# Kernel optimization log

Hardware: AMD Instinct MI355X
Metric: run time of the kernel (lower is better)

Reference implementation:

```python
import jax, jax.numpy as jnp
import numpy as np

B, S, E, H = 8, 1024, 1024, 16
D = E // H


def setup_inputs() -> dict:
    key = jax.random.key(0)
    ks = jax.random.split(key, 5)
    s = 1.0 / np.sqrt(E)
    return {
        "hidden_states": jax.random.normal(ks[0], (B, S, E), dtype=jnp.float32),
        "w_q": jax.random.normal(ks[1], (E, E), dtype=jnp.float32) * s,
        "w_k": jax.random.normal(ks[2], (E, E), dtype=jnp.float32) * s,
        "w_v": jax.random.normal(ks[3], (E, E), dtype=jnp.float32) * s,
        "w_out": jax.random.normal(ks[4], (E, E), dtype=jnp.float32) * s,
        "b_out": jnp.zeros((E,), dtype=jnp.float32),
    }


def reference(hidden_states, w_q, w_k, w_v, w_out, b_out):
    b, s = hidden_states.shape[0], hidden_states.shape[1]
    # Linear projections (weights stored as [in, out] = torch W^T)
    q = hidden_states @ w_q
    k = hidden_states @ w_k
    v = hidden_states @ w_v
    # Faithful to the original: raw reshape (B,S,E)->(B,H,S,D), NOT a head-split transpose
    q = q.reshape(b, H, s, D)
    k = k.reshape(b, H, s, D)
    v = v.reshape(b, H, s, D)
    # Scores scaled by embedding_size**-0.5 (original quirk, not head_dim**-0.5)
    scores = jnp.einsum("bhsd,bhtd->bhst", q, k) * (E ** -0.5)
    attn = jax.nn.softmax(scores, axis=-1)
    out = jnp.einsum("bhst,bhtd->bhsd", attn, v)  # [B,H,S,D]
    out = out.transpose(0, 2, 1, 3).reshape(b, s, E)  # [B,S,E]
    return out @ w_out + b_out
```

## Files before the change

### kernel.cpp

```cpp
#include <hip/hip_runtime.h>
#include <hip/hip_bf16.h>
#include <stdint.h>
#include <stddef.h>

static constexpr int Bb = 8, Ss = 1024, Ee = 1024, Hh = 16, Dd = 64;
static constexpr int Mm = Bb * Ss;

typedef __attribute__((ext_vector_type(8))) short frag8;
typedef __attribute__((ext_vector_type(4))) float fx4;
typedef __attribute__((ext_vector_type(4))) short s4v;

#define GP(p) ((const __attribute__((address_space(1))) void*)(p))
#define LP(p) ((__attribute__((address_space(3))) void*)(p))

static constexpr float QSC = 0.045084220027780106f;

__device__ inline short f2bf(float x) {
  union { float f; unsigned u; } c; c.f = x;
  unsigned u = c.u;
  unsigned r = (u + 0x7FFFu + ((u >> 16) & 1u)) >> 16;
  return (short)r;
}

__global__ __launch_bounds__(256) void cvt_kernel(const float* __restrict__ in,
                                                  short* __restrict__ out, int n4) {
  int i = blockIdx.x * 256 + threadIdx.x;
  if (i >= n4) return;
  float4 v = *((const float4*)in + i);
  union { short s[4]; uint2 u; } o;
  o.s[0] = f2bf(v.x); o.s[1] = f2bf(v.y); o.s[2] = f2bf(v.z); o.s[3] = f2bf(v.w);
  *(uint2*)(out + (size_t)i * 4) = o.u;
}

__global__ __launch_bounds__(256) void transpose_cvt4(const float* __restrict__ w0,
                                                      const float* __restrict__ w1,
                                                      const float* __restrict__ w2,
                                                      const float* __restrict__ w3,
                                                      short* __restrict__ WtBase) {
  __shared__ short tile[32][33];
  const int z = blockIdx.z;
  const float* W = z == 0 ? w0 : (z == 1 ? w1 : (z == 2 ? w2 : w3));
  short* Wt = WtBase + (size_t)z * 1024 * 1024;
  const int bx = blockIdx.x * 32;
  const int by = blockIdx.y * 32;
  const int tx = threadIdx.x & 31, ty = threadIdx.x >> 5;
  #pragma unroll
  for (int j = 0; j < 32; j += 8)
    tile[ty + j][tx] = f2bf(W[(size_t)(by + ty + j) * 1024 + bx + tx]);
  __syncthreads();
  #pragma unroll
  for (int j = 0; j < 32; j += 8)
    Wt[(size_t)(bx + ty + j) * 1024 + by + tx] = tile[tx][ty + j];
}

__global__ __launch_bounds__(256) void transpose_v(const short* __restrict__ V,
                                                   short* __restrict__ Vt) {
  __shared__ short tile[64][65];
  const int bh = blockIdx.y;
  const int s0 = blockIdx.x * 64;
  const short* Vb = V + (size_t)bh * 65536;
  short* Vtb = Vt + (size_t)bh * 65536;
  const int tx = threadIdx.x & 63, ty = threadIdx.x >> 6;
  #pragma unroll
  for (int j = 0; j < 64; j += 4)
    tile[ty + j][tx] = Vb[(size_t)(s0 + ty + j) * 64 + tx];
  __syncthreads();
  #pragma unroll
  for (int j = 0; j < 64; j += 4)
    Vtb[(size_t)(ty + j) * 1024 + s0 + tx] = tile[tx][ty + j];
}

template <int MODE>
__global__ __launch_bounds__(256) void gemm_bt(const short* __restrict__ A,
                                               const short* __restrict__ Bt,
                                               void* __restrict__ C0,
                                               void* __restrict__ C1,
                                               void* __restrict__ C2,
                                               const float* __restrict__ bias,
                                               int M, int N, int K) {
  __shared__ short As[128 * 32];
  __shared__ short Bs[128 * 32];
  const int t = threadIdx.x;
  const int w = t >> 6, lane = t & 63;
  const int fm = lane & 15, quad = lane >> 4;
  const int m0 = blockIdx.y * 128, n0 = blockIdx.x * 128;
  const int wm = (w >> 1) * 64, wn = (w & 1) * 64;
  fx4 acc[4][4];
  #pragma unroll
  for (int i = 0; i < 4; ++i)
    #pragma unroll
    for (int j = 0; j < 4; ++j) acc[i][j] = (fx4){0.f, 0.f, 0.f, 0.f};

  for (int k0 = 0; k0 < K; k0 += 32) {
    #pragma unroll
    for (int i = 0; i < 2; ++i) {
      int chunk = i * 256 + t;
      int row = chunk >> 2, cc = chunk & 3;
      __builtin_amdgcn_global_load_lds(GP(A + (size_t)(m0 + row) * K + k0 + cc * 8),
                                       LP(As + chunk * 8), 16, 0, 0);
      __builtin_amdgcn_global_load_lds(GP(Bt + (size_t)(n0 + row) * K + k0 + cc * 8),
                                       LP(Bs + chunk * 8), 16, 0, 0);
    }
    __syncthreads();
    frag8 af[4], bf[4];
    #pragma unroll
    for (int mt = 0; mt < 4; ++mt)
      af[mt] = *(const frag8*)(As + (wm + mt * 16 + fm) * 32 + quad * 8);
    #pragma unroll
    for (int nt = 0; nt < 4; ++nt)
      bf[nt] = *(const frag8*)(Bs + (wn + nt * 16 + fm) * 32 + quad * 8);
    #pragma unroll
    for (int mt = 0; mt < 4; ++mt)
      #pragma unroll
      for (int nt = 0; nt < 4; ++nt)
        acc[mt][nt] = __builtin_amdgcn_mfma_f32_16x16x32_bf16(af[mt], bf[nt], acc[mt][nt], 0, 0, 0);
    __syncthreads();
  }
  if (MODE == 0) {
    const int nb = n0 >> 10;
    short* dst = nb == 0 ? (short*)C0 : (nb == 1 ? (short*)C1 : (short*)C2);
    const float scl = (nb == 0) ? QSC : 1.0f;
    const int nl0 = n0 & 1023;
    #pragma unroll
    for (int mt = 0; mt < 4; ++mt)
      #pragma unroll
      for (int nt = 0; nt < 4; ++nt)
        #pragma unroll
        for (int r = 0; r < 4; ++r) {
          int row = m0 + wm + mt * 16 + quad * 4 + r;
          int col = nl0 + wn + nt * 16 + fm;
          dst[(size_t)row * 1024 + col] = f2bf(acc[mt][nt][r] * scl);
        }
  } else {
    #pragma unroll
    for (int mt = 0; mt < 4; ++mt)
      #pragma unroll
      for (int nt = 0; nt < 4; ++nt)
        #pragma unroll
        for (int r = 0; r < 4; ++r) {
          int row = m0 + wm + mt * 16 + quad * 4 + r;
          int col = n0 + wn + nt * 16 + fm;
          ((float*)C0)[(size_t)row * N + col] = acc[mt][nt][r] + bias[col];
        }
  }
}

__global__ __launch_bounds__(256, 2) void attn_kernel(const short* __restrict__ Q,
                                                      const short* __restrict__ K,
                                                      const short* __restrict__ Vt,
                                                      short* __restrict__ Ctx) {
  __shared__ short Ks[2][4096];
  __shared__ short Vs[2][4096];
  __shared__ short Plds[4 * 64 * 72];
  const int bh = blockIdx.x, qt = blockIdx.y;
  const int t = threadIdx.x;
  const int w = t >> 6, lane = t & 63;
  const int fm = lane & 15, quad = lane >> 4;
  const short* Qb = Q + (size_t)bh * 65536;
  const short* Kb = K + (size_t)bh * 65536;
  const short* Vb = Vt + (size_t)bh * 65536;
  const int q0 = qt * 256 + w * 64;
  short* myP = Plds + w * 4608;

  frag8 qb[4][2];
  #pragma unroll
  for (int g = 0; g < 4; ++g)
    #pragma unroll
    for (int h = 0; h < 2; ++h)
      qb[g][h] = *(const frag8*)(Qb + (size_t)(q0 + g * 16 + fm) * 64 + h * 32 + quad * 8);

  fx4 O[4][4];
  #pragma unroll
  for (int g = 0; g < 4; ++g)
    #pragma unroll
    for (int nt = 0; nt < 4; ++nt) O[g][nt] = (fx4){0.f, 0.f, 0.f, 0.f};
  float lp[4] = {0.f, 0.f, 0.f, 0.f};

  int koff[2], voff[2], loff[2];
  #pragma unroll
  for (int i = 0; i < 2; ++i) {
    int c = i * 256 + t;
    int cf = c & 15, cq = (c >> 4) & 3, ch = (c >> 6) & 1, cg = c >> 7;
    koff[i] = (cg * 16 + cf) * 64 + ch * 32 + cq * 8;
    voff[i] = (cg * 16 + cf) * 1024 + ch * 32 + cq * 8;
    loff[i] = c * 8;
  }

  #pragma unroll
  for (int i = 0; i < 2; ++i) {
    __builtin_amdgcn_global_load_lds(GP(Kb + koff[i]), LP(&Ks[0][0] + loff[i]), 16, 0, 0);
    __builtin_amdgcn_global_load_lds(GP(Vb + voff[i]), LP(&Vs[0][0] + loff[i]), 16, 0, 0);
  }
  __syncthreads();

  for (int c = 0; c < 16; ++c) {
    const int cur = c & 1;
    if (c < 15) {
      const int key0n = (c + 1) * 64;
      #pragma unroll
      for (int i = 0; i < 2; ++i) {
        __builtin_amdgcn_global_load_lds(GP(Kb + (size_t)key0n * 64 + koff[i]),
                                         LP(&Ks[cur ^ 1][0] + loff[i]), 16, 0, 0);
        __builtin_amdgcn_global_load_lds(GP(Vb + (size_t)key0n + voff[i]),
                                         LP(&Vs[cur ^ 1][0] + loff[i]), 16, 0, 0);
      }
    }
    const short* Kc = &Ks[cur][0];
    const short* Vc = &Vs[cur][0];

    #pragma unroll
    for (int s = 0; s < 4; ++s) {
      frag8 k0 = *(const frag8*)(Kc + (s * 2 + 0) * 512 + lane * 8);
      frag8 k1 = *(const frag8*)(Kc + (s * 2 + 1) * 512 + lane * 8);
      #pragma unroll
      for (int g = 0; g < 4; ++g) {
        fx4 z = (fx4){0.f, 0.f, 0.f, 0.f};
        z = __builtin_amdgcn_mfma_f32_16x16x32_bf16(k0, qb[g][0], z, 0, 0, 0);
        z = __builtin_amdgcn_mfma_f32_16x16x32_bf16(k1, qb[g][1], z, 0, 0, 0);
        s4v pv;
        #pragma unroll
        for (int r = 0; r < 4; ++r) {
          float p = __builtin_amdgcn_exp2f(z[r]);
          lp[g] += p;
          union { float f; unsigned u; } cv; cv.f = p;
          pv[r] = (short)(cv.u >> 16);
        }
        *(s4v*)(myP + (g * 16 + fm) * 72 + s * 16 + quad * 4) = pv;
      }
    }
    asm volatile("s_waitcnt lgkmcnt(0)" ::: "memory");
    #pragma unroll
    for (int h = 0; h < 2; ++h) {
      frag8 pf[4];
      #pragma unroll
      for (int g = 0; g < 4; ++g)
        pf[g] = *(const frag8*)(myP + (g * 16 + fm) * 72 + h * 32 + quad * 8);
      #pragma unroll
      for (int nt = 0; nt < 4; ++nt) {
        frag8 vf = *(const frag8*)(Vc + (nt * 2 + h) * 512 + lane * 8);
        #pragma unroll
        for (int g = 0; g < 4; ++g)
          O[g][nt] = __builtin_amdgcn_mfma_f32_16x16x32_bf16(pf[g], vf, O[g][nt], 0, 0, 0);
      }
    }
    __syncthreads();
  }

  float rl[4][4];
  #pragma unroll
  for (int g = 0; g < 4; ++g) {
    float v = lp[g];
    v += __shfl_xor(v, 16, 64);
    v += __shfl_xor(v, 32, 64);
    float inv = 1.f / v;
    #pragma unroll
    for (int r = 0; r < 4; ++r) rl[g][r] = __shfl(inv, quad * 4 + r, 16);
  }
  const int b = bh >> 4, h = bh & 15;
  #pragma unroll
  for (int g = 0; g < 4; ++g)
    #pragma unroll
    for (int nt = 0; nt < 4; ++nt)
      #pragma unroll
      for (int r = 0; r < 4; ++r) {
        int row = b * 1024 + q0 + g * 16 + quad * 4 + r;
        int col = h * 64 + nt * 16 + fm;
        Ctx[(size_t)row * 1024 + col] = f2bf(O[g][nt][r] * rl[g][r]);
      }
}

extern "C" void kernel_launch(void* const* d_in, const int* in_sizes, int n_in,
                              void* d_out, int out_size, void* d_ws, size_t ws_size,
                              hipStream_t stream) {
  const float* hs = (const float*)d_in[0];
  const float* wq = (const float*)d_in[1];
  const float* wk = (const float*)d_in[2];
  const float* wv = (const float*)d_in[3];
  const float* wo = (const float*)d_in[4];
  const float* bo = (const float*)d_in[5];
  float* out = (float*)d_out;

  char* wp = (char*)d_ws;
  const size_t MB16 = (size_t)Mm * Ee * 2;
  const size_t MB2  = (size_t)Ee * Ee * 2;
  short* Xb  = (short*)wp; wp += MB16;
  short* Wqt = (short*)wp; wp += MB2;
  short* Wkt = (short*)wp; wp += MB2;
  short* Wvt = (short*)wp; wp += MB2;
  short* Wot = (short*)wp; wp += MB2;
  short* Qb  = (short*)wp; wp += MB16;
  short* Kb  = (short*)wp; wp += MB16;
  short* Vb  = (short*)wp; wp += MB16;
  short* Vt  = (short*)wp; wp += MB16;
  short* Ctx = (short*)wp; wp += MB16;

  cvt_kernel<<<(Mm * Ee / 4 + 255) / 256, 256, 0, stream>>>(hs, Xb, Mm * Ee / 4);
  transpose_cvt4<<<dim3(32, 32, 4), 256, 0, stream>>>(wq, wk, wv, wo, Wqt);
  gemm_bt<0><<<dim3(24, 64), 256, 0, stream>>>(Xb, Wqt, Qb, Kb, Vb, nullptr, Mm, 3072, Ee);
  transpose_v<<<dim3(16, 128), 256, 0, stream>>>(Vb, Vt);
  attn_kernel<<<dim3(128, 4), 256, 0, stream>>>(Qb, Kb, Vt, Ctx);
  gemm_bt<1><<<dim3(8, 64), 256, 0, stream>>>(Ctx, Wot, out, nullptr, nullptr, bo, Mm, Ee, Ee);
}
```

Before: 251.2 us.

## Replace QKV projection GEMM with 256x256 double-buffered phased MFMA kernel

Adds a dedicated QKV projection kernel that uses 256x256 tiles, 512 threads and K=64 steps. Global-to-LDS loads are double-buffered and the next tile's prefetch is split across four MFMA phases with explicit vmcnt waits and barriers. It also applies an XOR swizzle to the LDS layout to avoid bank conflicts, remaps workgroups in groups of 8 for cache locality, and raises priority during MFMA bursts. The aim is to hide global memory latency and increase reuse per tile. In exchange it uses more LDS and registers per block, and correctness depends on the hand-tuned waitcnt counts.

```diff
diff --git a/kernel.cpp b/kernel.cpp
--- a/kernel.cpp
+++ b/kernel.cpp
@@ -68,6 +68,145 @@
   #pragma unroll
   for (int j = 0; j < 64; j += 4)
     Vtb[(size_t)(ty + j) * 1024 + s0 + tx] = tile[tx][ty + j];
+}
+
+__global__ __launch_bounds__(512, 2) void gemm_qkv_8ph(const short* __restrict__ A,
+                                                       const short* __restrict__ Bt,
+                                                       short* __restrict__ Cq,
+                                                       short* __restrict__ Ck,
+                                                       short* __restrict__ Cv) {
+  __shared__ short As[2][16384];
+  __shared__ short Bs[2][16384];
+  const int t = threadIdx.x;
+  const int w = t >> 6, lane = t & 63;
+  const int fm = lane & 15, quad = lane >> 4;
+  const int wm = w >> 1, wn = w & 1;
+  const int wg = (blockIdx.x & 7) * 48 + (blockIdx.x >> 3);
+  const int nt_i = wg % 12, mt_i = wg / 12;
+  const int m0 = mt_i * 256, n0 = nt_i * 256;
+
+  int goffA[4], goffB[4];
+  #pragma unroll
+  for (int i = 0; i < 4; ++i) {
+    int c = i * 512 + t, row = c >> 3, col8 = (c & 7) ^ (row & 7);
+    goffA[i] = row * 1024 + col8 * 8;
+  }
+  {
+    int row32 = (t >> 3) & 31, hv = t >> 8, col8 = (t & 7) ^ (row32 & 7);
+    #pragma unroll
+    for (int j = 0; j < 4; ++j)
+      goffB[j] = (hv * 128 + j * 32 + row32) * 1024 + col8 * 8;
+  }
+  const short* Ag = A + (size_t)m0 * 1024;
+  const short* Bg = Bt + (size_t)n0 * 1024;
+
+  fx4 acc[4][8];
+  #pragma unroll
+  for (int i = 0; i < 4; ++i)
+    #pragma unroll
+    for (int j = 0; j < 8; ++j) acc[i][j] = (fx4){0.f, 0.f, 0.f, 0.f};
+
+  const int s0o = ((0 * 4 + quad) ^ (fm & 7)) * 8;
+  const int s1o = ((1 * 4 + quad) ^ (fm & 7)) * 8;
+  const int aBase = (wm * 64 + fm) * 64;
+  const int bBase = wn * 2048 + fm * 64;
+
+#define STG_A(i, koff, dstbuf) \
+  __builtin_amdgcn_global_load_lds(GP(Ag + (koff) + goffA[i]), \
+                                   LP((dstbuf) + ((i) * 512 + t) * 8), 16, 0, 0)
+#define STG_B(j, koff, dstbuf) \
+  __builtin_amdgcn_global_load_lds(GP(Bg + (koff) + goffB[j]), \
+                                   LP((dstbuf) + ((j) * 512 + t) * 8), 16, 0, 0)
+#define LOAD_B(p) \
+  { const short* bp = Bb + (p) * 4096 + bBase; \
+    bf[0][0] = *(const frag8*)(bp + s0o); \
+    bf[0][1] = *(const frag8*)(bp + s1o); \
+    bf[1][0] = *(const frag8*)(bp + 1024 + s0o); \
+    bf[1][1] = *(const frag8*)(bp + 1024 + s1o); }
+#define MFMA_PH(p) \
+  __builtin_amdgcn_s_barrier(); \
+  asm volatile("s_waitcnt lgkmcnt(0)" ::: "memory"); \
+  __builtin_amdgcn_s_setprio(1); \
+  _Pragma("unroll") \
+  for (int mf = 0; mf < 4; ++mf) { \
+    acc[mf][2*(p)]   = __builtin_amdgcn_mfma_f32_16x16x32_bf16(af[mf][0], bf[0][0], acc[mf][2*(p)],   0, 0, 0); \
+    acc[mf][2*(p)]   = __builtin_amdgcn_mfma_f32_16x16x32_bf16(af[mf][1], bf[0][1], acc[mf][2*(p)],   0, 0, 0); \
+    acc[mf][2*(p)+1] = __builtin_amdgcn_mfma_f32_16x16x32_bf16(af[mf][0], bf[1][0], acc[mf][2*(p)+1], 0, 0, 0); \
+    acc[mf][2*(p)+1] = __builtin_amdgcn_mfma_f32_16x16x32_bf16(af[mf][1], bf[1][1], acc[mf][2*(p)+1], 0, 0, 0); \
+  } \
+  __builtin_amdgcn_s_setprio(0);
+
+  #pragma unroll
+  for (int i = 0; i < 4; ++i) STG_A(i, 0, &As[0][0]);
+  #pragma unroll
+  for (int j = 0; j < 4; ++j) STG_B(j, 0, &Bs[0][0]);
+  asm volatile("s_waitcnt vmcnt(3)" ::: "memory");
+  __builtin_amdgcn_s_barrier();
+
+  for (int kt = 0; kt < 16; ++kt) {
+    const short* Ab = As[kt & 1];
+    const short* Bb = Bs[kt & 1];
+    short* An = (short*)As[(kt & 1) ^ 1];
+    short* Bn = (short*)Bs[(kt & 1) ^ 1];
+    const int kn = (kt + 1) * 64;
+    const bool pf = kt < 15;
+    frag8 af[4][2], bf[2][2];
+
+    #pragma unroll
+    for (int mf = 0; mf < 4; ++mf) {
+      const short* ap = Ab + aBase + mf * 1024;
+      af[mf][0] = *(const frag8*)(ap + s0o);
+      af[mf][1] = *(const frag8*)(ap + s1o);
+    }
+    LOAD_B(0);
+    if (pf) { STG_A(0, kn, An); STG_A(1, kn, An); }
+    MFMA_PH(0);
+    if (pf) asm volatile("s_waitcnt vmcnt(4)" ::: "memory");
+    else    asm volatile("s_waitcnt vmcnt(2)" ::: "memory");
+    __builtin_amdgcn_s_barrier();
+
+    LOAD_B(1);
+    if (pf) { STG_A(2, kn, An); STG_A(3, kn, An); }
+    MFMA_PH(1);
+    if (pf) asm volatile("s_waitcnt vmcnt(5)" ::: "memory");
+    else    asm volatile("s_waitcnt vmcnt(1)" ::: "memory");
+    __builtin_amdgcn_s_barrier();
+
+    LOAD_B(2);
+    if (pf) { STG_B(0, kn, Bn); STG_B(1, kn, Bn); }
+    MFMA_PH(2);
+    if (pf) asm volatile("s_waitcnt vmcnt(6)" ::: "memory");
+    else    asm volatile("s_waitcnt vmcnt(0)" ::: "memory");
+    __builtin_amdgcn_s_barrier();
+
+    LOAD_B(3);
+    if (pf) { STG_B(2, kn, Bn); STG_B(3, kn, Bn); }
+    MFMA_PH(3);
+    if (pf) {
+      asm volatile("s_waitcnt vmcnt(3)" ::: "memory");
+      __builtin_amdgcn_s_barrier();
+    }
+  }
+#undef STG_A
+#undef STG_B
+#undef LOAD_B
+#undef MFMA_PH
+
+  const int nb = n0 >> 10;
+  short* dst = nb == 0 ? Cq : (nb == 1 ? Ck : Cv);
+  const float scl = (nb == 0) ? QSC : 1.0f;
+  const int nl0 = (n0 & 1023) + wn * 128;
+  const int rbase = m0 + wm * 64 + quad * 4;
+  #pragma unroll
+  for (int mf = 0; mf < 4; ++mf)
+    #pragma unroll
+    for (int nf = 0; nf < 8; ++nf)
+      #pragma unroll
+      for (int r = 0; r < 4; ++r) {
+        int row = rbase + mf * 16 + r;
+        int col = nl0 + nf * 16 + fm;
+        dst[(size_t)row * 1024 + col] = f2bf(acc[mf][nf][r] * scl);
+      }
 }
 
 template <int MODE>
@@ -102,47 +241,30 @@
                                        LP(Bs + chunk * 8), 16, 0, 0);
     }
     __syncthreads();
-    frag8 af[4], bf[4];
+    frag8 af[4], bfr[4];
     #pragma unroll
     for (int mt = 0; mt < 4; ++mt)
       af[mt] = *(const frag8*)(As + (wm + mt * 16 + fm) * 32 + quad * 8);
     #pragma unroll
     for (int nt = 0; nt < 4; ++nt)
-      bf[nt] = *(const frag8*)(Bs + (wn + nt * 16 + fm) * 32 + quad * 8);
+      bfr[nt] = *(const frag8*)(Bs + (wn + nt * 16 + fm) * 32 + quad * 8);
     #pragma unroll
     for (int mt = 0; mt < 4; ++mt)
       #pragma unroll
       for (int nt = 0; nt < 4; ++nt)
-        acc[mt][nt] = __builtin_amdgcn_mfma_f32_16x16x32_bf16(af[mt], bf[nt], acc[mt][nt], 0, 0, 0);
+        acc[mt][nt] = __builtin_amdgcn_mfma_f32_16x16x32_bf16(af[mt], bfr[nt], acc[mt][nt], 0, 0, 0);
     __syncthreads();
   }
-  if (MODE == 0) {
-    const int nb = n0 >> 10;
-    short* dst = nb == 0 ? (short*)C0 : (nb == 1 ? (short*)C1 : (short*)C2);
-    const float scl = (nb == 0) ? QSC : 1.0f;
-    const int nl0 = n0 & 1023;
-    #pragma unroll
-    for (int mt = 0; mt < 4; ++mt)
-      #pragma unroll
-      for (int nt = 0; nt < 4; ++nt)
-        #pragma unroll
-        for (int r = 0; r < 4; ++r) {
-          int row = m0 + wm + mt * 16 + quad * 4 + r;
-          int col = nl0 + wn + nt * 16 + fm;
-          dst[(size_t)row * 1024 + col] = f2bf(acc[mt][nt][r] * scl);
-        }
-  } else {
-    #pragma unroll
-    for (int mt = 0; mt < 4; ++mt)
-      #pragma unroll
-      for (int nt = 0; nt < 4; ++nt)
-        #pragma unroll
-        for (int r = 0; r < 4; ++r) {
-          int row = m0 + wm + mt * 16 + quad * 4 + r;
-          int col = n0 + wn + nt * 16 + fm;
-          ((float*)C0)[(size_t)row * N + col] = acc[mt][nt][r] + bias[col];
-        }
-  }
+  #pragma unroll
+  for (int mt = 0; mt < 4; ++mt)
+    #pragma unroll
+    for (int nt = 0; nt < 4; ++nt)
+      #pragma unroll
+      for (int r = 0; r < 4; ++r) {
+        int row = m0 + wm + mt * 16 + quad * 4 + r;
+        int col = n0 + wn + nt * 16 + fm;
+        ((float*)C0)[(size_t)row * N + col] = acc[mt][nt][r] + bias[col];
+      }
 }
 
 __global__ __launch_bounds__(256, 2) void attn_kernel(const short* __restrict__ Q,
@@ -296,7 +418,7 @@
 
   cvt_kernel<<<(Mm * Ee / 4 + 255) / 256, 256, 0, stream>>>(hs, Xb, Mm * Ee / 4);
   transpose_cvt4<<<dim3(32, 32, 4), 256, 0, stream>>>(wq, wk, wv, wo, Wqt);
-  gemm_bt<0><<<dim3(24, 64), 256, 0, stream>>>(Xb, Wqt, Qb, Kb, Vb, nullptr, Mm, 3072, Ee);
+  gemm_qkv_8ph<<<384, 512, 0, stream>>>(Xb, Wqt, Qb, Kb, Vb);
   transpose_v<<<dim3(16, 128), 256, 0, stream>>>(Vb, Vt);
   attn_kernel<<<dim3(128, 4), 256, 0, stream>>>(Qb, Kb, Vt, Ctx);
   gemm_bt<1><<<dim3(8, 64), 256, 0, stream>>>(Ctx, Wot, out, nullptr, nullptr, bo, Mm, Ee, Ee);
```

Result: faster. 241.0 us (-4.1%).
